# Kernel tuning notes

Measured on AMD Instinct MI355X. Metric: run time of the kernel, lower is better.

## Reference

```python
import jax, jax.numpy as jnp
import numpy as np

D = 512      # d_model
H = 8        # num_heads
DK = D // H  # d_k = 64
S = 1024     # seq_len
B = 4        # batch
LW = 64      # local_window
SR = 0.8     # sparsity_ratio -> keep k = int(S*(1-SR)) = 204
PD = 64      # pattern_dim
NP = 8       # num_patterns
NEG = -1e9


def setup_inputs() -> dict:
    k = jax.random.key(0)
    ks = jax.random.split(k, 24)
    s = 0.02
    def lin(ki, fan_in, fan_out):
        return jax.random.normal(ki, (fan_in, fan_out), jnp.float32) * s
    return {
        'query': jax.random.normal(ks[0], (B, S, D), jnp.float32),
        'key':   jax.random.normal(ks[1], (B, S, D), jnp.float32),
        'value': jax.random.normal(ks[2], (B, S, D), jnp.float32),
        'wq': lin(ks[3], D, D), 'bq': jnp.zeros((D,), jnp.float32),
        'wk': lin(ks[4], D, D), 'bk': jnp.zeros((D,), jnp.float32),
        'wv': lin(ks[5], D, D), 'bv': jnp.zeros((D,), jnp.float32),
        'wo': lin(ks[6], D, D), 'bo': jnp.zeros((D,), jnp.float32),
        'pw1': lin(ks[7], D, PD), 'pb1': jnp.zeros((PD,), jnp.float32),
        'pw2': lin(ks[8], PD, PD), 'pb2': jnp.zeros((PD,), jnp.float32),
        'pattern_bank': jax.random.normal(ks[9], (NP, PD), jnp.float32) * 0.1,
        'pattern_gate': jnp.ones((NP,), jnp.float32) / NP,
    }


def _make_mask(scores3):
    """Faithful vectorization of MaskGenerator. scores3: (B,S,S) full-dim QK scores."""
    k_top = max(1, int(S * (1.0 - SR)))
    # local window mask: row i attends to cols [max(0,i-LW//2), min(S,i+LW//2))
    idx = jnp.arange(S)
    local = ((idx[None, :] >= idx[:, None] - LW // 2) &
             (idx[None, :] < idx[:, None] + LW // 2)).astype(jnp.float32)  # (S,S)
    # global mask: importance = mean over heads of expanded scores == scores3
    _, top3 = jax.lax.top_k(scores3, k_top)  # (B,S,k)
    g3 = jnp.zeros((B, S, S), jnp.float32).at[
        jnp.arange(B)[:, None, None], jnp.arange(S)[None, :, None], top3].set(1.0)
    # random sparsification mask (fixed key -> deterministic reference)
    rnd = (jax.random.uniform(jax.random.key(42), (B, H, S, S)) < (1.0 - SR)).astype(jnp.float32)
    combined = (local[None, None] + g3[:, None] + rnd) > 0  # (B,H,S,S) bool
    # ensure sparsity: per-row top-k of masked scores
    scores4 = jnp.broadcast_to(scores3[:, None], (B, H, S, S))
    masked_scores = scores4 * combined.astype(scores4.dtype)
    _, top4 = jax.lax.top_k(masked_scores, k_top)  # (B,H,S,k)
    final = jnp.zeros((B, H, S, S), jnp.float32).at[
        jnp.arange(B)[:, None, None, None],
        jnp.arange(H)[None, :, None, None],
        jnp.arange(S)[None, None, :, None],
        top4].set(1.0)
    return final


def reference(query, key, value, wq, bq, wk, bk, wv, bv, wo, bo,
              pw1, pb1, pw2, pb2, pattern_bank, pattern_gate):
    # PatternLearner
    enc = jnp.tanh(jax.nn.relu(query @ pw1 + pb1) @ pw2 + pb2)        # (B,S,PD)
    pattern_scores = enc @ pattern_bank.T / jnp.sqrt(jnp.float32(PD))  # (B,S,NP)
    pattern_probs = jax.nn.softmax(pattern_scores, axis=-1)            # temperature=1
    weighted_patterns = pattern_probs * pattern_gate[None, None, :]
    # full-dim QK scores used for mask generation (as in SparseAttentionModule.forward)
    Qf = query @ wq + bq
    Kf = key @ wk + bk
    scores3 = jnp.einsum('bid,bjd->bij', Qf, Kf) / jnp.sqrt(jnp.float32(DK))
    attention_mask = _make_mask(scores3)  # (B,H,S,S) float {0,1}
    # AttentionOptimizer (non-flash path, eval -> dropout off)
    Qh = Qf.reshape(B, S, H, DK).transpose(0, 2, 1, 3)
    Kh = Kf.reshape(B, S, H, DK).transpose(0, 2, 1, 3)
    Vh = (value @ wv + bv).reshape(B, S, H, DK).transpose(0, 2, 1, 3)
    scores = jnp.einsum('bhid,bhjd->bhij', Qh, Kh) / jnp.sqrt(jnp.float32(DK))
    scores = jnp.where(attention_mask > 0, scores, NEG)
    attn = jax.nn.softmax(scores, axis=-1)
    out = jnp.einsum('bhij,bhjd->bhid', attn, Vh)
    out = out.transpose(0, 2, 1, 3).reshape(B, S, D)
    attention_output = out @ wo + bo
    return attention_output, attention_mask, weighted_patterns
```

## Files before the change

### kernel.cpp

```cpp
#include <hip/hip_runtime.h>
#include <hip/hip_bf16.h>
#include <hip/hip_fp16.h>
#include <math.h>

#define BB   4
#define SSQ  1024
#define DDM  512
#define HHD  8
#define KTOP 204
#define NPAT 8
#define PDIM 64

typedef unsigned long long u64;
typedef unsigned int u32;
typedef unsigned short u16;

__device__ __forceinline__ float ldin(const void* p, size_t i, int f32) {
    if (f32) return ((const float*)p)[i];
    u16 h = ((const u16*)p)[i];
    return __uint_as_float(((u32)h) << 16);
}

__device__ __forceinline__ float bf2f(u16 h) {
    return __uint_as_float(((u32)h) << 16);
}

typedef _Float16 hf2v __attribute__((ext_vector_type(2)));
union H2U { u32 u; hf2v v; __half2 h; };

__device__ __forceinline__ u32 packh2(float a, float b) {
    H2U c; c.h = __floats2half2_rn(a, b); return c.u;
}

__device__ __forceinline__ float fdot2f(u32 a, u32 b, float c) {
#if __has_builtin(__builtin_amdgcn_fdot2)
    H2U ua, ub; ua.u = a; ub.u = b;
    return __builtin_amdgcn_fdot2(ua.v, ub.v, c, false);
#else
    H2U ua, ub; ua.u = a; ub.u = b;
    float2 fa = __half22float2(ua.h), fb = __half22float2(ub.h);
    return fmaf(fa.y, fb.y, fmaf(fa.x, fb.x, c));
#endif
}

union U8H { uint4 u; _Float16 h[8]; };

__global__ __launch_bounds__(64)
void detect_kernel(const void* q, int* flag) {
    int lane = threadIdx.x;
    const u16* p = (const u16*)q;
    int good = 0;
    #pragma unroll
    for (int k = 0; k < 4; ++k) {
        int i = (lane * 4 + k) * 2;
        float v = __uint_as_float(((u32)p[i]) << 16);
        float a = fabsf(v);
        if (a > 0.00390625f && a < 64.f) ++good;
    }
    #pragma unroll
    for (int off = 32; off >= 1; off >>= 1) good += __shfl_xor(good, off);
    if (lane == 0) *flag = (good < 128) ? 1 : 0;
}

__global__ __launch_bounds__(64)
void pattern_kernel(const void* __restrict__ q,
                    const void* __restrict__ pw1, const void* __restrict__ pb1,
                    const void* __restrict__ pw2, const void* __restrict__ pb2,
                    const void* __restrict__ bank, const void* __restrict__ gate,
                    const int* __restrict__ flagp,
                    float* __restrict__ out2) {
    __shared__ float qs[DDM];
    __shared__ float h1[PDIM];
    __shared__ float enc[PDIM];
    __shared__ float ps[NPAT];
    int f32 = *flagp;
    int row = blockIdx.x;
    int t = threadIdx.x;
    for (int i = t; i < DDM; i += 64) qs[i] = ldin(q, (size_t)row * DDM + i, f32);
    __syncthreads();
    float a0 = ldin(pb1, t, f32), a1 = 0.f, a2 = 0.f, a3 = 0.f;
    #pragma unroll 4
    for (int d = 0; d < DDM; d += 4) {
        a0 = fmaf(qs[d + 0], ldin(pw1, (size_t)(d + 0) * PDIM + t, f32), a0);
        a1 = fmaf(qs[d + 1], ldin(pw1, (size_t)(d + 1) * PDIM + t, f32), a1);
        a2 = fmaf(qs[d + 2], ldin(pw1, (size_t)(d + 2) * PDIM + t, f32), a2);
        a3 = fmaf(qs[d + 3], ldin(pw1, (size_t)(d + 3) * PDIM + t, f32), a3);
    }
    h1[t] = fmaxf((a0 + a1) + (a2 + a3), 0.f);
    __syncthreads();
    float acc2 = ldin(pb2, t, f32);
    for (int d = 0; d < PDIM; ++d) acc2 = fmaf(h1[d], ldin(pw2, (size_t)d * PDIM + t, f32), acc2);
    enc[t] = tanhf(acc2);
    __syncthreads();
    if (t < NPAT) {
        float a = 0.f;
        for (int d = 0; d < PDIM; ++d) a = fmaf(enc[d], ldin(bank, (size_t)t * PDIM + d, f32), a);
        ps[t] = a * 0.125f;
    }
    __syncthreads();
    if (t < NPAT) {
        float m = ps[0];
        for (int n = 1; n < NPAT; ++n) m = fmaxf(m, ps[n]);
        float sum = 0.f;
        for (int n = 0; n < NPAT; ++n) sum += expf(ps[n] - m);
        float e = expf(ps[t] - m);
        out2[(size_t)row * NPAT + t] = e / sum * ldin(gate, t, f32);
    }
}

__global__ __launch_bounds__(256, 4)
void projf_kernel(const void* __restrict__ query, const void* __restrict__ key,
                  const void* __restrict__ value,
                  const void* __restrict__ wq, const void* __restrict__ bq,
                  const void* __restrict__ wk, const void* __restrict__ bk,
                  const void* __restrict__ wv, const void* __restrict__ bv,
                  const int* __restrict__ flagp,
                  float* __restrict__ Qf32, float* __restrict__ Kf32, float* __restrict__ Vf32,
                  u16* __restrict__ Khf, u16* __restrict__ Vhf) {
    __shared__ float Xs[64][68];
    __shared__ float Ws[64][68];
    int f32 = *flagp;
    int z = blockIdx.z;
    const void* X = (z == 0) ? query : ((z == 1) ? key : value);
    const void* W = (z == 0) ? wq : ((z == 1) ? wk : wv);
    const void* Bv = (z == 0) ? bq : ((z == 1) ? bk : bv);
    float* Y = (z == 0) ? Qf32 : ((z == 1) ? Kf32 : Vf32);
    int c0 = blockIdx.x * 64, r0 = blockIdx.y * 64;
    int tx = threadIdx.x & 15, ty = threadIdx.x >> 4;

    int sr[4], sq[4];
    #pragma unroll
    for (int it = 0; it < 4; ++it) {
        int idx = threadIdx.x + it * 256;
        sr[it] = idx >> 4;
        sq[it] = idx & 15;
    }

    float4 xr[4], wr[4];
    if (f32) {
        #pragma unroll
        for (int it = 0; it < 4; ++it) {
            xr[it] = *reinterpret_cast<const float4*>((const float*)X + (size_t)(r0 + sr[it]) * DDM + sq[it] * 4);
            wr[it] = *reinterpret_cast<const float4*>((const float*)W + (size_t)sr[it] * DDM + c0 + sq[it] * 4);
        }
    } else {
        #pragma unroll
        for (int it = 0; it < 4; ++it) {
            ushort4 xh = *reinterpret_cast<const ushort4*>((const u16*)X + (size_t)(r0 + sr[it]) * DDM + sq[it] * 4);
            ushort4 wh = *reinterpret_cast<const ushort4*>((const u16*)W + (size_t)sr[it] * DDM + c0 + sq[it] * 4);
            xr[it] = make_float4(bf2f(xh.x), bf2f(xh.y), bf2f(xh.z), bf2f(xh.w));
            wr[it] = make_float4(bf2f(wh.x), bf2f(wh.y), bf2f(wh.z), bf2f(wh.w));
        }
    }

    float acc[4][4] = {};
    for (int k0 = 0; k0 < DDM; k0 += 64) {
        __syncthreads();
        #pragma unroll
        for (int it = 0; it < 4; ++it) {
            *reinterpret_cast<float4*>(&Xs[sr[it]][sq[it] * 4]) = xr[it];
            *reinterpret_cast<float4*>(&Ws[sr[it]][sq[it] * 4]) = wr[it];
        }
        __syncthreads();
        int kn = k0 + 64;
        if (kn < DDM) {
            if (f32) {
                #pragma unroll
                for (int it = 0; it < 4; ++it) {
                    xr[it] = *reinterpret_cast<const float4*>((const float*)X + (size_t)(r0 + sr[it]) * DDM + kn + sq[it] * 4);
                    wr[it] = *reinterpret_cast<const float4*>((const float*)W + (size_t)(kn + sr[it]) * DDM + c0 + sq[it] * 4);
                }
            } else {
                #pragma unroll
                for (int it = 0; it < 4; ++it) {
                    ushort4 xh = *reinterpret_cast<const ushort4*>((const u16*)X + (size_t)(r0 + sr[it]) * DDM + kn + sq[it] * 4);
                    ushort4 wh = *reinterpret_cast<const ushort4*>((const u16*)W + (size_t)(kn + sr[it]) * DDM + c0 + sq[it] * 4);
                    xr[it] = make_float4(bf2f(xh.x), bf2f(xh.y), bf2f(xh.z), bf2f(xh.w));
                    wr[it] = make_float4(bf2f(wh.x), bf2f(wh.y), bf2f(wh.z), bf2f(wh.w));
                }
            }
        }
        #pragma unroll 4
        for (int kk = 0; kk < 64; kk += 4) {
            float4 xv[4];
            #pragma unroll
            for (int a = 0; a < 4; ++a)
                xv[a] = *reinterpret_cast<const float4*>(&Xs[ty + 16 * a][kk]);
            #pragma unroll
            for (int j = 0; j < 4; ++j) {
                float4 wv = *reinterpret_cast<const float4*>(&Ws[kk + j][4 * tx]);
                #pragma unroll
                for (int a = 0; a < 4; ++a) {
                    float x = ((const float*)&xv[a])[j];
                    acc[a][0] = fmaf(x, wv.x, acc[a][0]);
                    acc[a][1] = fmaf(x, wv.y, acc[a][1]);
                    acc[a][2] = fmaf(x, wv.z, acc[a][2]);
                    acc[a][3] = fmaf(x, wv.w, acc[a][3]);
                }
            }
        }
    }
    #pragma unroll
    for (int a = 0; a < 4; ++a) {
        int r = r0 + ty + 16 * a;
        float4 o;
        o.x = acc[a][0] + ldin(Bv, c0 + 4 * tx + 0, f32);
        o.y = acc[a][1] + ldin(Bv, c0 + 4 * tx + 1, f32);
        o.z = acc[a][2] + ldin(Bv, c0 + 4 * tx + 2, f32);
        o.w = acc[a][3] + ldin(Bv, c0 + 4 * tx + 3, f32);
        *reinterpret_cast<float4*>(&Y[(size_t)r * DDM + c0 + 4 * tx]) = o;
        if (z != 0) {
            uint2 ph;
            ph.x = packh2(o.x, o.y);
            ph.y = packh2(o.z, o.w);
            u16* dst = (z == 1) ? Khf : Vhf;
            *reinterpret_cast<uint2*>(&dst[(size_t)r * DDM + c0 + 4 * tx]) = ph;
        }
    }
}

__global__ __launch_bounds__(256, 2)
void scoresf_kernel(const float* __restrict__ Qf32, const float* __restrict__ Kf32,
                    float* __restrict__ S3f) {
    __shared__ float Qs[128][68];
    __shared__ float Ks[64][68];
    int b = blockIdx.z;
    const float* Qb = Qf32 + (size_t)b * SSQ * DDM;
    const float* Kb = Kf32 + (size_t)b * SSQ * DDM;
    float* S3 = S3f + (size_t)b * SSQ * SSQ;
    int j0 = blockIdx.x * 64, i0 = blockIdx.y * 128;
    int tx = threadIdx.x & 15, ty = threadIdx.x >> 4;

    int qr_r[8], qr_s[8], kr_r[4], kr_s[4];
    #pragma unroll
    for (int it = 0; it < 8; ++it) {
        int idx = threadIdx.x + it * 256;
        qr_r[it] = idx >> 4;
        qr_s[it] = idx & 15;
    }
    #pragma unroll
    for (int it = 0; it < 4; ++it) {
        int idx = threadIdx.x + it * 256;
        kr_r[it] = idx >> 4;
        kr_s[it] = idx & 15;
    }

    float4 qr[8], kr[4];
    #pragma unroll
    for (int it = 0; it < 8; ++it)
        qr[it] = *reinterpret_cast<const float4*>(Qb + (size_t)(i0 + qr_r[it]) * DDM + qr_s[it] * 4);
    #pragma unroll
    for (int it = 0; it < 4; ++it)
        kr[it] = *reinterpret_cast<const float4*>(Kb + (size_t)(j0 + kr_r[it]) * DDM + kr_s[it] * 4);

    float acc[8][4] = {};
    for (int k0 = 0; k0 < DDM; k0 += 64) {
        __syncthreads();
        #pragma unroll
        for (int it = 0; it < 8; ++it)
            *reinterpret_cast<float4*>(&Qs[qr_r[it]][qr_s[it] * 4]) = qr[it];
        #pragma unroll
        for (int it = 0; it < 4; ++it)
            *reinterpret_cast<float4*>(&Ks[kr_r[it]][kr_s[it] * 4]) = kr[it];
        __syncthreads();
        int kn = k0 + 64;
        if (kn < DDM) {
            #pragma unroll
            for (int it = 0; it < 8; ++it)
                qr[it] = *reinterpret_cast<const float4*>(Qb + (size_t)(i0 + qr_r[it]) * DDM + kn + qr_s[it] * 4);
            #pragma unroll
            for (int it = 0; it < 4; ++it)
                kr[it] = *reinterpret_cast<const float4*>(Kb + (size_t)(j0 + kr_r[it]) * DDM + kn + kr_s[it] * 4);
        }
        #pragma unroll 2
        for (int kk = 0; kk < 64; kk += 4) {
            float4 qv[8], kv[4];
            #pragma unroll
            for (int a = 0; a < 8; ++a)
                qv[a] = *reinterpret_cast<const float4*>(&Qs[ty + 16 * a][kk]);
            #pragma unroll
            for (int b2 = 0; b2 < 4; ++b2)
                kv[b2] = *reinterpret_cast<const float4*>(&Ks[tx + 16 * b2][kk]);
            #pragma unroll
            for (int a = 0; a < 8; ++a)
                #pragma unroll
                for (int b2 = 0; b2 < 4; ++b2) {
                    acc[a][b2] = fmaf(qv[a].x, kv[b2].x, acc[a][b2]);
                    acc[a][b2] = fmaf(qv[a].y, kv[b2].y, acc[a][b2]);
                    acc[a][b2] = fmaf(qv[a].z, kv[b2].z, acc[a][b2]);
                    acc[a][b2] = fmaf(qv[a].w, kv[b2].w, acc[a][b2]);
                }
        }
    }
    __syncthreads();
    #pragma unroll
    for (int a = 0; a < 8; ++a)
        #pragma unroll
        for (int b2 = 0; b2 < 4; ++b2)
            Qs[ty + 16 * a][tx + 16 * b2] = acc[a][b2] * 0.125f;
    __syncthreads();
    #pragma unroll
    for (int it = 0; it < 8; ++it) {
        int row = qr_r[it], q4 = qr_s[it];
        float4 o = *reinterpret_cast<const float4*>(&Qs[row][q4 * 4]);
        *reinterpret_cast<float4*>(&S3[(size_t)(i0 + row) * SSQ + j0 + q4 * 4]) = o;
    }
}

__global__ __launch_bounds__(256)
void maskselect_kernel(const float* __restrict__ S3f,
                       u64* __restrict__ bitmask,
                       u16* __restrict__ lists) {
    __shared__ u32 keys[1024];
    __shared__ u32 sel[1024];
    __shared__ u32 hist[256];
    __shared__ u32 ssum[256];
    __shared__ u32 scan[256];
    __shared__ u32 pick_digit, pick_rem;
    int i = blockIdx.x, b = blockIdx.y;
    int t = threadIdx.x;
    const float* srow = S3f + (size_t)b * SSQ * SSQ + (size_t)i * SSQ;
    for (int j = t; j < 1024; j += 256) {
        u32 bits = __float_as_uint(srow[j]);
        keys[j] = (bits & 0x80000000u) ? ~bits : (bits | 0x80000000u);
    }
    __syncthreads();
    u32 prefix = 0, himask = 0, rem = KTOP;
    for (int p = 3; p >= 0; --p) {
        int shift = p * 8;
        hist[t] = 0;
        __syncthreads();
        for (int j = t; j < 1024; j += 256) {
            u32 kb = keys[j];
            if ((kb & himask) == prefix) atomicAdd(&hist[(kb >> shift) & 0xFFu], 1u);
        }
        __syncthreads();
        ssum[t] = hist[t];
        __syncthreads();
        for (int off = 1; off < 256; off <<= 1) {
            u32 v = (t + off < 256) ? ssum[t + off] : 0u;
            __syncthreads();
            ssum[t] += v;
            __syncthreads();
        }
        u32 nxt = (t < 255) ? ssum[t + 1] : 0u;
        if (ssum[t] >= rem && nxt < rem) { pick_digit = (u32)t; pick_rem = rem - nxt; }
        __syncthreads();
        prefix |= pick_digit << shift;
        rem = pick_rem;
        himask |= (0xFFu << shift);
        __syncthreads();
    }
    u32 vstar = prefix;
    u32 tneed = rem;
    u32 eq[4]; u32 local = 0;
    #pragma unroll
    for (int a = 0; a < 4; ++a) {
        int j = 4 * t + a;
        u32 kb = keys[j];
        sel[j] = (kb > vstar) ? 1u : 0u;
        eq[a] = (kb == vstar) ? 1u : 0u;
        local += eq[a];
    }
    scan[t] = local;
    __syncthreads();
    for (int off = 1; off < 256; off <<= 1) {
        u32 v = (t >= off) ? scan[t - off] : 0u;
        __syncthreads();
        scan[t] += v;
        __syncthreads();
    }
    u32 base = (t > 0) ? scan[t - 1] : 0u;
    #pragma unroll
    for (int a = 0; a < 4; ++a) {
        if (eq[a]) { if (base < tneed) sel[4 * t + a] = 1u; base += 1; }
    }
    __syncthreads();
    if (t < 16) {
        u64 wbits = 0;
        for (int l = 0; l < 64; ++l)
            if (sel[t * 64 + l]) wbits |= (1ull << l);
        bitmask[((size_t)b * SSQ + i) * 16 + t] = wbits;
    }
    u32 ones = sel[4 * t] + sel[4 * t + 1] + sel[4 * t + 2] + sel[4 * t + 3];
    scan[t] = ones;
    __syncthreads();
    for (int off = 1; off < 256; off <<= 1) {
        u32 v = (t >= off) ? scan[t - off] : 0u;
        __syncthreads();
        scan[t] += v;
        __syncthreads();
    }
    u32 pos = scan[t] - ones;
    u16* lrow = lists + ((size_t)b * SSQ + i) * 256;
    #pragma unroll
    for (int a = 0; a < 4; ++a) {
        if (sel[4 * t + a]) lrow[pos++] = (u16)(4 * t + a);
    }
    if (t < 52) lrow[KTOP + t] = 0;
}

__global__ __launch_bounds__(256, 8)
void attn_sparse_kernel(const float* __restrict__ Qf32, const u16* __restrict__ Khf,
                        const u16* __restrict__ Vhf, const u16* __restrict__ lists,
                        float* __restrict__ AO) {
    __shared__ float pbuf[4][256];
    __shared__ uint2 lraw[4][64];
    int lane = threadIdx.x & 63, w = threadIdx.x >> 6;
    int b = blockIdx.z, h = blockIdx.y, i = blockIdx.x * 4 + w;
    size_t qoff = ((size_t)(b * SSQ + i)) * DDM + h * 64;

    const uint2* Lrow = reinterpret_cast<const uint2*>(lists + ((size_t)(b * SSQ + i)) * 256);
    lraw[w][lane] = Lrow[lane];
    const u16* list = reinterpret_cast<const u16*>(lraw[w]);

    int sub = lane & 3;
    int g   = lane >> 2;
    u32 qh[8];
    {
        float4 qa = *reinterpret_cast<const float4*>(&Qf32[qoff + sub * 8]);
        float4 qb = *reinterpret_cast<const float4*>(&Qf32[qoff + sub * 8 + 4]);
        float4 qc = *reinterpret_cast<const float4*>(&Qf32[qoff + 32 + sub * 8]);
        float4 qd = *reinterpret_cast<const float4*>(&Qf32[qoff + 32 + sub * 8 + 4]);
        qh[0] = packh2(qa.x, qa.y); qh[1] = packh2(qa.z, qa.w);
        qh[2] = packh2(qb.x, qb.y); qh[3] = packh2(qb.z, qb.w);
        qh[4] = packh2(qc.x, qc.y); qh[5] = packh2(qc.z, qc.w);
        qh[6] = packh2(qd.x, qd.y); qh[7] = packh2(qd.z, qd.w);
    }

    const u16* Kb = Khf + (size_t)b * SSQ * DDM + h * 64 + sub * 8;
    float m = -1e30f;
    for (int base = 0; base < KTOP; base += 16) {
        int idx = base + g;
        int valid = (idx < KTOP);
        int j = valid ? (int)list[idx] : 0;
        const u16* kr = Kb + (size_t)j * DDM;
        uint4 k0 = *reinterpret_cast<const uint4*>(kr);
        uint4 k1 = *reinterpret_cast<const uint4*>(kr + 32);
        float p = fdot2f(qh[0], k0.x, 0.f);
        p = fdot2f(qh[1], k0.y, p);
        p = fdot2f(qh[2], k0.z, p);
        p = fdot2f(qh[3], k0.w, p);
        p = fdot2f(qh[4], k1.x, p);
        p = fdot2f(qh[5], k1.y, p);
        p = fdot2f(qh[6], k1.z, p);
        p = fdot2f(qh[7], k1.w, p);
        p += __shfl_xor(p, 1);
        p += __shfl_xor(p, 2);
        float s = valid ? p * 0.125f : -1e30f;
        m = fmaxf(m, s);
        if (valid && sub == 0) pbuf[w][idx] = s;
    }
    #pragma unroll
    for (int off = 32; off >= 1; off >>= 1) m = fmaxf(m, __shfl_xor(m, off));

    float lsum = 0.f;
    for (int idx = lane; idx < KTOP; idx += 64) {
        float p = expf(pbuf[w][idx] - m);
        pbuf[w][idx] = p;
        lsum += p;
    }
    #pragma unroll
    for (int off = 32; off >= 1; off >>= 1) lsum += __shfl_xor(lsum, off);

    int vg = lane >> 3, vl = lane & 7;
    const u16* Vb = Vhf + (size_t)b * SSQ * DDM + h * 64 + vl * 8;
    float ac[8] = {};
    #pragma unroll 2
    for (int tt = 0; tt < KTOP; tt += 8) {
        int e = tt + vg;
        if (e < KTOP) {
            int j = (int)list[e];
            float pwt = pbuf[w][e];
            U8H vv;
            vv.u = *reinterpret_cast<const uint4*>(Vb + (size_t)j * DDM);
            ac[0] = fmaf((float)vv.h[0], pwt, ac[0]);
            ac[1] = fmaf((float)vv.h[1], pwt, ac[1]);
            ac[2] = fmaf((float)vv.h[2], pwt, ac[2]);
            ac[3] = fmaf((float)vv.h[3], pwt, ac[3]);
            ac[4] = fmaf((float)vv.h[4], pwt, ac[4]);
            ac[5] = fmaf((float)vv.h[5], pwt, ac[5]);
            ac[6] = fmaf((float)vv.h[6], pwt, ac[6]);
            ac[7] = fmaf((float)vv.h[7], pwt, ac[7]);
        }
    }
    #pragma unroll
    for (int off = 8; off <= 32; off <<= 1) {
        #pragma unroll
        for (int t = 0; t < 8; ++t) ac[t] += __shfl_xor(ac[t], off);
    }
    if (vg == 0) {
        float inv = 1.0f / lsum;
        float4 o0, o1;
        o0.x = ac[0] * inv; o0.y = ac[1] * inv; o0.z = ac[2] * inv; o0.w = ac[3] * inv;
        o1.x = ac[4] * inv; o1.y = ac[5] * inv; o1.z = ac[6] * inv; o1.w = ac[7] * inv;
        *reinterpret_cast<float4*>(&AO[qoff + vl * 8]) = o0;
        *reinterpret_cast<float4*>(&AO[qoff + vl * 8 + 4]) = o1;
    }
}

__global__ __launch_bounds__(256, 4)
void outproj_kernel(const float* __restrict__ AO, const void* __restrict__ wo,
                    const void* __restrict__ bo, const int* __restrict__ flagp,
                    float* __restrict__ out0) {
    __shared__ float Xs[64][68];
    __shared__ float Ws[64][68];
    int f32 = *flagp;
    int c0 = blockIdx.x * 64, r0 = blockIdx.y * 64;
    int tx = threadIdx.x & 15, ty = threadIdx.x >> 4;

    int sr[4], sq[4];
    #pragma unroll
    for (int it = 0; it < 4; ++it) {
        int idx = threadIdx.x + it * 256;
        sr[it] = idx >> 4;
        sq[it] = idx & 15;
    }

    float4 xr[4], wr[4];
    #pragma unroll
    for (int it = 0; it < 4; ++it)
        xr[it] = *reinterpret_cast<const float4*>(AO + (size_t)(r0 + sr[it]) * DDM + sq[it] * 4);
    if (f32) {
        #pragma unroll
        for (int it = 0; it < 4; ++it)
            wr[it] = *reinterpret_cast<const float4*>((const float*)wo + (size_t)sr[it] * DDM + c0 + sq[it] * 4);
    } else {
        #pragma unroll
        for (int it = 0; it < 4; ++it) {
            ushort4 wh = *reinterpret_cast<const ushort4*>((const u16*)wo + (size_t)sr[it] * DDM + c0 + sq[it] * 4);
            wr[it] = make_float4(bf2f(wh.x), bf2f(wh.y), bf2f(wh.z), bf2f(wh.w));
        }
    }

    float acc[4][4] = {};
    for (int k0 = 0; k0 < DDM; k0 += 64) {
        __syncthreads();
        #pragma unroll
        for (int it = 0; it < 4; ++it) {
            *reinterpret_cast<float4*>(&Xs[sr[it]][sq[it] * 4]) = xr[it];
            *reinterpret_cast<float4*>(&Ws[sr[it]][sq[it] * 4]) = wr[it];
        }
        __syncthreads();
        int kn = k0 + 64;
        if (kn < DDM) {
            #pragma unroll
            for (int it = 0; it < 4; ++it)
                xr[it] = *reinterpret_cast<const float4*>(AO + (size_t)(r0 + sr[it]) * DDM + kn + sq[it] * 4);
            if (f32) {
                #pragma unroll
                for (int it = 0; it < 4; ++it)
                    wr[it] = *reinterpret_cast<const float4*>((const float*)wo + (size_t)(kn + sr[it]) * DDM + c0 + sq[it] * 4);
            } else {
                #pragma unroll
                for (int it = 0; it < 4; ++it) {
                    ushort4 wh = *reinterpret_cast<const ushort4*>((const u16*)wo + (size_t)(kn + sr[it]) * DDM + c0 + sq[it] * 4);
                    wr[it] = make_float4(bf2f(wh.x), bf2f(wh.y), bf2f(wh.z), bf2f(wh.w));
                }
            }
        }
        #pragma unroll 4
        for (int kk = 0; kk < 64; kk += 4) {
            float4 xv[4];
            #pragma unroll
            for (int a = 0; a < 4; ++a)
                xv[a] = *reinterpret_cast<const float4*>(&Xs[ty + 16 * a][kk]);
            #pragma unroll
            for (int j = 0; j < 4; ++j) {
                float4 wv = *reinterpret_cast<const float4*>(&Ws[kk + j][4 * tx]);
                #pragma unroll
                for (int a = 0; a < 4; ++a) {
                    float x = ((const float*)&xv[a])[j];
                    acc[a][0] = fmaf(x, wv.x, acc[a][0]);
                    acc[a][1] = fmaf(x, wv.y, acc[a][1]);
                    acc[a][2] = fmaf(x, wv.z, acc[a][2]);
                    acc[a][3] = fmaf(x, wv.w, acc[a][3]);
                }
            }
        }
    }
    #pragma unroll
    for (int a = 0; a < 4; ++a) {
        int r = r0 + ty + 16 * a;
        float4 o;
        o.x = acc[a][0] + ldin(bo, c0 + 4 * tx + 0, f32);
        o.y = acc[a][1] + ldin(bo, c0 + 4 * tx + 1, f32);
        o.z = acc[a][2] + ldin(bo, c0 + 4 * tx + 2, f32);
        o.w = acc[a][3] + ldin(bo, c0 + 4 * tx + 3, f32);
        *reinterpret_cast<float4*>(&out0[(size_t)r * DDM + c0 + 4 * tx]) = o;
    }
}

__global__ __launch_bounds__(256)
void maskwrite_kernel(const u64* __restrict__ bitmask,
                      float* __restrict__ out1) {
    int row = blockIdx.x;
    int t = threadIdx.x;
    int b = row >> 10, i = row & 1023;
    const u64* mb = bitmask + (size_t)row * 16;
    int j0 = t * 4;
    u64 w0 = mb[j0 >> 6];
    float4 v4;
    v4.x = ((w0 >> (j0 & 63)) & 1ull) ? 1.0f : 0.0f;
    v4.y = ((w0 >> ((j0 + 1) & 63)) & 1ull) ? 1.0f : 0.0f;
    v4.z = ((w0 >> ((j0 + 2) & 63)) & 1ull) ? 1.0f : 0.0f;
    v4.w = ((w0 >> ((j0 + 3) & 63)) & 1ull) ? 1.0f : 0.0f;
    for (int h = 0; h < HHD; ++h) {
        size_t base_o = (((size_t)b * HHD + h) * SSQ + i) * SSQ;
        *reinterpret_cast<float4*>(out1 + base_o + (size_t)t * 4) = v4;
    }
}

extern "C" void kernel_launch(void* const* d_in, const int* in_sizes, int n_in,
                              void* d_out, int out_size, void* d_ws, size_t ws_size,
                              hipStream_t stream) {
    const void* query = d_in[0];
    const void* key   = d_in[1];
    const void* value = d_in[2];
    const void* wq = d_in[3];  const void* bq = d_in[4];
    const void* wk = d_in[5];  const void* bk = d_in[6];
    const void* wv = d_in[7];  const void* bv = d_in[8];
    const void* wo = d_in[9];  const void* bo = d_in[10];
    const void* pw1 = d_in[11]; const void* pb1 = d_in[12];
    const void* pw2 = d_in[13]; const void* pb2 = d_in[14];
    const void* pattern_bank = d_in[15];
    const void* pattern_gate = d_in[16];

    float* out0 = (float*)d_out;
    float* out1 = out0 + (size_t)BB * SSQ * DDM;
    float* out2 = out1 + (size_t)BB * HHD * SSQ * SSQ;

    int* flag = (int*)d_ws;
    u64* bitmask = (u64*)((char*)d_ws + 65536);

    char* SCR = (char*)out1;
    float* Qf32 = (float*)(SCR);
    float* Kf32 = (float*)(SCR + (8ull << 20));
    float* Vf32 = (float*)(SCR + (16ull << 20));
    float* AO   = (float*)(SCR + (24ull << 20));
    float* S3f  = (float*)(SCR + (32ull << 20));
    u16*   Khf  = (u16*)  (SCR + (48ull << 20));
    u16*   Vhf  = (u16*)  (SCR + (52ull << 20));
    u16*   lists= (u16*)  (SCR + (56ull << 20));

    detect_kernel<<<dim3(1), dim3(64), 0, stream>>>(query, flag);

    pattern_kernel<<<dim3(BB * SSQ), dim3(64), 0, stream>>>(
        query, pw1, pb1, pw2, pb2, pattern_bank, pattern_gate, flag, out2);

    projf_kernel<<<dim3(DDM / 64, BB * SSQ / 64, 3), dim3(256), 0, stream>>>(
        query, key, value, wq, bq, wk, bk, wv, bv, flag, Qf32, Kf32, Vf32, Khf, Vhf);

    scoresf_kernel<<<dim3(SSQ / 64, SSQ / 128, BB), dim3(256), 0, stream>>>(
        Qf32, Kf32, S3f);

    maskselect_kernel<<<dim3(SSQ, BB), dim3(256), 0, stream>>>(S3f, bitmask, lists);

    attn_sparse_kernel<<<dim3(SSQ / 4, HHD, BB), dim3(256), 0, stream>>>(
        Qf32, Khf, Vhf, lists, AO);

    outproj_kernel<<<dim3(DDM / 64, BB * SSQ / 64), dim3(256), 0, stream>>>(
        AO, wo, bo, flag, out0);

    maskwrite_kernel<<<dim3(BB * SSQ), dim3(256), 0, stream>>>(bitmask, out1);
}
```

Baseline: 574.8 us.

## Enlarge scores GEMM tile to 128x128 with XOR-swizzled LDS layout

The full-dimension QK scores kernel now computes a 128x128 output tile per block instead of 128x64, giving each thread an 8x8 register accumulator. The padded shared-memory arrays are replaced by an unpadded buffer with an XOR swizzle to avoid bank conflicts, and that buffer is reused for the output staging. The aim is more reuse of each loaded K element and fewer global loads per FLOP. In exchange, register pressure rises, occupancy drops to one block per SM, and the grid is halved to 256 blocks.

```diff
diff --git a/kernel.cpp b/kernel.cpp
--- a/kernel.cpp
+++ b/kernel.cpp
@@ -44,6 +44,8 @@
 }
 
 union U8H { uint4 u; _Float16 h[8]; };
+
+#define SWZ(r, c) ((c) ^ (((r) & 7) << 2))
 
 __global__ __launch_bounds__(64)
 void detect_kernel(const void* q, int* flag) {
@@ -219,72 +221,69 @@
     }
 }
 
-__global__ __launch_bounds__(256, 2)
+__global__ __launch_bounds__(256, 1)
 void scoresf_kernel(const float* __restrict__ Qf32, const float* __restrict__ Kf32,
                     float* __restrict__ S3f) {
-    __shared__ float Qs[128][68];
-    __shared__ float Ks[64][68];
+    __shared__ float LDSbuf[16384];
+    float (*Qs)[64] = reinterpret_cast<float(*)[64]>(LDSbuf);
+    float (*Ks)[64] = reinterpret_cast<float(*)[64]>(LDSbuf + 8192);
     int b = blockIdx.z;
     const float* Qb = Qf32 + (size_t)b * SSQ * DDM;
     const float* Kb = Kf32 + (size_t)b * SSQ * DDM;
     float* S3 = S3f + (size_t)b * SSQ * SSQ;
-    int j0 = blockIdx.x * 64, i0 = blockIdx.y * 128;
+    int j0 = blockIdx.x * 128, i0 = blockIdx.y * 128;
     int tx = threadIdx.x & 15, ty = threadIdx.x >> 4;
 
-    int qr_r[8], qr_s[8], kr_r[4], kr_s[4];
+    int sr_[8], ss_[8];
     #pragma unroll
     for (int it = 0; it < 8; ++it) {
         int idx = threadIdx.x + it * 256;
-        qr_r[it] = idx >> 4;
-        qr_s[it] = idx & 15;
-    }
-    #pragma unroll
-    for (int it = 0; it < 4; ++it) {
-        int idx = threadIdx.x + it * 256;
-        kr_r[it] = idx >> 4;
-        kr_s[it] = idx & 15;
-    }
-
-    float4 qr[8], kr[4];
-    #pragma unroll
-    for (int it = 0; it < 8; ++it)
-        qr[it] = *reinterpret_cast<const float4*>(Qb + (size_t)(i0 + qr_r[it]) * DDM + qr_s[it] * 4);
-    #pragma unroll
-    for (int it = 0; it < 4; ++it)
-        kr[it] = *reinterpret_cast<const float4*>(Kb + (size_t)(j0 + kr_r[it]) * DDM + kr_s[it] * 4);
-
-    float acc[8][4] = {};
+        sr_[it] = idx >> 4;
+        ss_[it] = idx & 15;
+    }
+
+    float4 qr[8], kr[8];
+    #pragma unroll
+    for (int it = 0; it < 8; ++it) {
+        qr[it] = *reinterpret_cast<const float4*>(Qb + (size_t)(i0 + sr_[it]) * DDM + ss_[it] * 4);
+        kr[it] = *reinterpret_cast<const float4*>(Kb + (size_t)(j0 + sr_[it]) * DDM + ss_[it] * 4);
+    }
+
+    float acc[8][8] = {};
     for (int k0 = 0; k0 < DDM; k0 += 64) {
         __syncthreads();
         #pragma unroll
-        for (int it = 0; it < 8; ++it)
-            *reinterpret_cast<float4*>(&Qs[qr_r[it]][qr_s[it] * 4]) = qr[it];
-        #pragma unroll
-        for (int it = 0; it < 4; ++it)
-            *reinterpret_cast<float4*>(&Ks[kr_r[it]][kr_s[it] * 4]) = kr[it];
+        for (int it = 0; it < 8; ++it) {
+            int r = sr_[it];
+            *reinterpret_cast<float4*>(&Qs[r][SWZ(r, ss_[it] * 4)]) = qr[it];
+            *reinterpret_cast<float4*>(&Ks[r][SWZ(r, ss_[it] * 4)]) = kr[it];
+        }
         __syncthreads();
         int kn = k0 + 64;
         if (kn < DDM) {
             #pragma unroll
-            for (int it = 0; it < 8; ++it)
-                qr[it] = *reinterpret_cast<const float4*>(Qb + (size_t)(i0 + qr_r[it]) * DDM + kn + qr_s[it] * 4);
-            #pragma unroll
-            for (int it = 0; it < 4; ++it)
-                kr[it] = *reinterpret_cast<const float4*>(Kb + (size_t)(j0 + kr_r[it]) * DDM + kn + kr_s[it] * 4);
-        }
-        #pragma unroll 2
+            for (int it = 0; it < 8; ++it) {
+                qr[it] = *reinterpret_cast<const float4*>(Qb + (size_t)(i0 + sr_[it]) * DDM + kn + ss_[it] * 4);
+                kr[it] = *reinterpret_cast<const float4*>(Kb + (size_t)(j0 + sr_[it]) * DDM + kn + ss_[it] * 4);
+            }
+        }
+        #pragma unroll 1
         for (int kk = 0; kk < 64; kk += 4) {
-            float4 qv[8], kv[4];
-            #pragma unroll
-            for (int a = 0; a < 8; ++a)
-                qv[a] = *reinterpret_cast<const float4*>(&Qs[ty + 16 * a][kk]);
-            #pragma unroll
-            for (int b2 = 0; b2 < 4; ++b2)
-                kv[b2] = *reinterpret_cast<const float4*>(&Ks[tx + 16 * b2][kk]);
+            float4 qv[8], kv[8];
+            #pragma unroll
+            for (int a = 0; a < 8; ++a) {
+                int r = ty + 16 * a;
+                qv[a] = *reinterpret_cast<const float4*>(&Qs[r][SWZ(r, kk)]);
+            }
+            #pragma unroll
+            for (int b2 = 0; b2 < 8; ++b2) {
+                int r = tx + 16 * b2;
+                kv[b2] = *reinterpret_cast<const float4*>(&Ks[r][SWZ(r, kk)]);
+            }
             #pragma unroll
             for (int a = 0; a < 8; ++a)
                 #pragma unroll
-                for (int b2 = 0; b2 < 4; ++b2) {
+                for (int b2 = 0; b2 < 8; ++b2) {
                     acc[a][b2] = fmaf(qv[a].x, kv[b2].x, acc[a][b2]);
                     acc[a][b2] = fmaf(qv[a].y, kv[b2].y, acc[a][b2]);
                     acc[a][b2] = fmaf(qv[a].z, kv[b2].z, acc[a][b2]);
@@ -293,17 +292,19 @@
         }
     }
     __syncthreads();
+    float (*Os)[128] = reinterpret_cast<float(*)[128]>(LDSbuf);
     #pragma unroll
     for (int a = 0; a < 8; ++a)
         #pragma unroll
-        for (int b2 = 0; b2 < 4; ++b2)
-            Qs[ty + 16 * a][tx + 16 * b2] = acc[a][b2] * 0.125f;
-    __syncthreads();
-    #pragma unroll
-    for (int it = 0; it < 8; ++it) {
-        int row = qr_r[it], q4 = qr_s[it];
-        float4 o = *reinterpret_cast<const float4*>(&Qs[row][q4 * 4]);
-        *reinterpret_cast<float4*>(&S3[(size_t)(i0 + row) * SSQ + j0 + q4 * 4]) = o;
+        for (int b2 = 0; b2 < 8; ++b2)
+            Os[ty + 16 * a][tx + 16 * b2] = acc[a][b2] * 0.125f;
+    __syncthreads();
+    #pragma unroll
+    for (int it = 0; it < 16; ++it) {
+        int idx = threadIdx.x + it * 256;
+        int row = idx >> 5, slot = idx & 31;
+        float4 o = *reinterpret_cast<const float4*>(&Os[row][slot * 4]);
+        *reinterpret_cast<float4*>(&S3[(size_t)(i0 + row) * SSQ + j0 + slot * 4]) = o;
     }
 }
 
@@ -651,7 +652,7 @@
     projf_kernel<<<dim3(DDM / 64, BB * SSQ / 64, 3), dim3(256), 0, stream>>>(
         query, key, value, wq, bq, wk, bk, wv, bv, flag, Qf32, Kf32, Vf32, Khf, Vhf);
 
-    scoresf_kernel<<<dim3(SSQ / 64, SSQ / 128, BB), dim3(256), 0, stream>>>(
+    scoresf_kernel<<<dim3(SSQ / 128, SSQ / 128, BB), dim3(256), 0, stream>>>(
         Qf32, Kf32, S3f);
 
     maskselect_kernel<<<dim3(SSQ, BB), dim3(256), 0, stream>>>(S3f, bitmask, lists);
```

Result: slower. 596.9 us (+3.8%).
